# Kernel optimization log

Measured on AMD Instinct MI355X. Metric: run time of the kernel, lower is better.

## Reference

```python
import jax, jax.numpy as jnp
import numpy as np

# Spike nonlinearity with straight-through surrogate gradient
# fwd: z = (v_scaled > 0); bwd: dz/dv = clamp(1 - |v_scaled|, min=0)
@jax.custom_vjp
def spike(v_scaled):
    return (v_scaled > 0).astype(v_scaled.dtype)

def _spike_fwd(v_scaled):
    return spike(v_scaled), v_scaled

def _spike_bwd(v_scaled, g):
    return (g * jnp.maximum(1.0 - jnp.abs(v_scaled), 0.0),)

spike.defvjp(_spike_fwd, _spike_bwd)

_H = np.array([-0.00285825, 0.09859432, 0.07954306, 0.08560576, 0.0910411, 0.10557652,
               0.04608637, 0.07096123, 0.01989892, 0.03412642, 0.03321506, 0.01300904,
               -0.02348068, 0.06102338, -0.00509757, 0.00051896], dtype=np.float32)
_D = np.array([0.04908372, -0.00948576, 0.00083943, 0.07961489, 0.08128168, 0.02395899,
               0.05197346, 0.01595683, 0.02185501, 0.01893722, 0.0074682, -0.00088913,
               0.01660369, 0.00298292, 0.0071363, 0.00279426], dtype=np.float32)
_T = np.array([0.20153396, -0.01304637, -0.19541621, 0.19903184, 0.1529713, -0.00479887,
               0.07102165, 0.02109929, 0.01368383, -0.00360851, -0.01454873, -0.03991705,
               -0.00440092, -0.06122432, -0.02989412, -0.04975629], dtype=np.float32)


def setup_inputs() -> dict:
    key = jax.random.key(0)
    x = jax.random.normal(key, (64, 1024, 1024), dtype=jnp.float32)
    return {
        "x": x,
        "h": jnp.asarray(_H),
        "d": jnp.asarray(_D),
        "T": jnp.asarray(_T),
    }


def reference(x, h, d, T):
    signs = jax.lax.stop_gradient(jnp.sign(x))  # detached in original
    x_abs = jnp.abs(x)

    def step(carry, hdT):
        v, z, out = carry
        ht, dt, Tt = hdT
        v = v - z * ht
        v_scaled = (v - Tt) / (jnp.abs(v) + 1.0)
        z = spike(v_scaled)
        out = out + z * dt
        return (v, z, out), None

    init = (x_abs, jnp.zeros_like(x_abs), jnp.zeros_like(x_abs))
    (_, _, out), _ = jax.lax.scan(step, init, (h, d, T))  # K=16 steps
    return out * signs
```

## Files before the change

kernel.cpp:

```cpp
#include <hip/hip_runtime.h>


__device__ __forceinline__ float snn_elem(float xe,
                                          const float* __restrict__ hh,
                                          const float* __restrict__ dd,
                                          const float* __restrict__ TT) {
    float v = fabsf(xe);
    float z   = (v > TT[0]) ? 1.0f : 0.0f;
    float acc = z * dd[0];
#pragma unroll
    for (int t = 1; t < 16; ++t) {
        v   = fmaf(-z, hh[t], v);
        z   = (v > TT[t]) ? 1.0f : 0.0f;
        acc = fmaf(z, dd[t], acc);
    }
    float s = (xe > 0.0f) ? 1.0f : ((xe < 0.0f) ? -1.0f : 0.0f);
    return acc * s;
}

__global__ __launch_bounds__(256) void snn_scan_kernel(
    const float* __restrict__ x,
    const float* __restrict__ h,
    const float* __restrict__ d,
    const float* __restrict__ T,
    float* __restrict__ out,
    int n4, int n) {
    float hh[16], dd[16], TT[16];
#pragma unroll
    for (int t = 0; t < 16; ++t) {
        hh[t] = h[t];
        dd[t] = d[t];
        TT[t] = T[t];
    }

    const int stride = gridDim.x * blockDim.x;
    const float4* __restrict__ x4 = reinterpret_cast<const float4*>(x);
    float4* __restrict__ o4       = reinterpret_cast<float4*>(out);

    for (int i = blockIdx.x * blockDim.x + threadIdx.x; i < n4; i += stride) {
        float4 xv = x4[i];
        float4 ov;
        ov.x = snn_elem(xv.x, hh, dd, TT);
        ov.y = snn_elem(xv.y, hh, dd, TT);
        ov.z = snn_elem(xv.z, hh, dd, TT);
        ov.w = snn_elem(xv.w, hh, dd, TT);
        o4[i] = ov;
    }

    for (int i = n4 * 4 + blockIdx.x * blockDim.x + threadIdx.x; i < n;
         i += stride) {
        out[i] = snn_elem(x[i], hh, dd, TT);
    }
}

extern "C" void kernel_launch(void* const* d_in, const int* in_sizes, int n_in,
                              void* d_out, int out_size, void* d_ws, size_t ws_size,
                              hipStream_t stream) {
    const float* x = (const float*)d_in[0];
    const float* h = (const float*)d_in[1];
    const float* d = (const float*)d_in[2];
    const float* T = (const float*)d_in[3];
    float* out     = (float*)d_out;

    const int n  = in_sizes[0];
    const int n4 = n / 4;

    const int block = 256;
    int grid = 2048;
    const int needed = (n4 + block - 1) / block;
    if (grid > needed) grid = needed > 0 ? needed : 1;

    snn_scan_kernel<<<grid, block, 0, stream>>>(x, h, d, T, out, n4, n);
}
```

Baseline: 144.6 us.

## Software-pipeline grid-stride loads with 4-deep prefetch and nontemporal stores

Restructures the grid-stride loop so each thread issues four float4 loads ahead and computes on the previous batch while the next loads are in flight. Outputs are written with nontemporal stores to avoid polluting cache. The sign multiply is replaced by a sign-bit XOR with a zero check. Adds register pressure and a separate tail path for elements outside the full-step region.

```diff
diff --git a/kernel.cpp b/kernel.cpp
--- a/kernel.cpp
+++ b/kernel.cpp
@@ -1,5 +1,7 @@
 #include <hip/hip_runtime.h>
 
+
+typedef float f32x4 __attribute__((ext_vector_type(4)));
 
 __device__ __forceinline__ float snn_elem(float xe,
                                           const float* __restrict__ hh,
@@ -14,8 +16,19 @@
         z   = (v > TT[t]) ? 1.0f : 0.0f;
         acc = fmaf(z, dd[t], acc);
     }
-    float s = (xe > 0.0f) ? 1.0f : ((xe < 0.0f) ? -1.0f : 0.0f);
-    return acc * s;
+    unsigned ai = __float_as_uint(acc) ^ (__float_as_uint(xe) & 0x80000000u);
+    float r = __uint_as_float(ai);
+    return (xe == 0.0f) ? 0.0f : r;
+}
+
+__device__ __forceinline__ f32x4 snn_vec4(f32x4 xv,
+                                          const float* __restrict__ hh,
+                                          const float* __restrict__ dd,
+                                          const float* __restrict__ TT) {
+    f32x4 ov;
+#pragma unroll
+    for (int e = 0; e < 4; ++e) ov[e] = snn_elem(xv[e], hh, dd, TT);
+    return ov;
 }
 
 __global__ __launch_bounds__(256) void snn_scan_kernel(
@@ -24,31 +37,47 @@
     const float* __restrict__ d,
     const float* __restrict__ T,
     float* __restrict__ out,
-    int n4, int n) {
+    int n4, int n4_full, int n) {
     float hh[16], dd[16], TT[16];
 #pragma unroll
-    for (int t = 0; t < 16; ++t) {
-        hh[t] = h[t];
-        dd[t] = d[t];
-        TT[t] = T[t];
+    for (int t = 0; t < 16; ++t) { hh[t] = h[t]; dd[t] = d[t]; TT[t] = T[t]; }
+
+    const f32x4* __restrict__ x4 = (const f32x4*)x;
+    f32x4* __restrict__ o4       = (f32x4*)out;
+
+    const int tid  = blockIdx.x * blockDim.x + threadIdx.x;
+    const int nt   = gridDim.x * blockDim.x;
+    const int step = nt * 4;
+
+    int base = tid;
+    if (base < n4_full) {
+        f32x4 c0 = x4[base];
+        f32x4 c1 = x4[base + nt];
+        f32x4 c2 = x4[base + 2 * nt];
+        f32x4 c3 = x4[base + 3 * nt];
+        int nb = base + step;
+        for (; nb < n4_full; nb += step) {
+            f32x4 p0 = x4[nb];
+            f32x4 p1 = x4[nb + nt];
+            f32x4 p2 = x4[nb + 2 * nt];
+            f32x4 p3 = x4[nb + 3 * nt];
+            __builtin_nontemporal_store(snn_vec4(c0, hh, dd, TT), o4 + base);
+            __builtin_nontemporal_store(snn_vec4(c1, hh, dd, TT), o4 + base + nt);
+            __builtin_nontemporal_store(snn_vec4(c2, hh, dd, TT), o4 + base + 2 * nt);
+            __builtin_nontemporal_store(snn_vec4(c3, hh, dd, TT), o4 + base + 3 * nt);
+            c0 = p0; c1 = p1; c2 = p2; c3 = p3;
+            base = nb;
+        }
+        __builtin_nontemporal_store(snn_vec4(c0, hh, dd, TT), o4 + base);
+        __builtin_nontemporal_store(snn_vec4(c1, hh, dd, TT), o4 + base + nt);
+        __builtin_nontemporal_store(snn_vec4(c2, hh, dd, TT), o4 + base + 2 * nt);
+        __builtin_nontemporal_store(snn_vec4(c3, hh, dd, TT), o4 + base + 3 * nt);
     }
 
-    const int stride = gridDim.x * blockDim.x;
-    const float4* __restrict__ x4 = reinterpret_cast<const float4*>(x);
-    float4* __restrict__ o4       = reinterpret_cast<float4*>(out);
-
-    for (int i = blockIdx.x * blockDim.x + threadIdx.x; i < n4; i += stride) {
-        float4 xv = x4[i];
-        float4 ov;
-        ov.x = snn_elem(xv.x, hh, dd, TT);
-        ov.y = snn_elem(xv.y, hh, dd, TT);
-        ov.z = snn_elem(xv.z, hh, dd, TT);
-        ov.w = snn_elem(xv.w, hh, dd, TT);
-        o4[i] = ov;
+    for (int i = n4_full + tid; i < n4; i += nt) {
+        __builtin_nontemporal_store(snn_vec4(x4[i], hh, dd, TT), o4 + i);
     }
-
-    for (int i = n4 * 4 + blockIdx.x * blockDim.x + threadIdx.x; i < n;
-         i += stride) {
+    for (int i = n4 * 4 + tid; i < n; i += nt) {
         out[i] = snn_elem(x[i], hh, dd, TT);
     }
 }
@@ -70,5 +99,9 @@
     const int needed = (n4 + block - 1) / block;
     if (grid > needed) grid = needed > 0 ? needed : 1;
 
-    snn_scan_kernel<<<grid, block, 0, stream>>>(x, h, d, T, out, n4, n);
+    const int nt      = grid * block;
+    const int step    = nt * 4;
+    const int n4_full = (n4 / step) * step;
+
+    snn_scan_kernel<<<grid, block, 0, stream>>>(x, h, d, T, out, n4, n4_full, n);
 }
```

Result: slower. 218.4 us (+51.1%).

## Replace per-element 16-step scan with piecewise-constant LUT built on device

Applied to the files above, without the earlier changes.

Adds a single-block kernel that finds every breakpoint in |x| where the 16-step spike pattern changes, by bisecting over float bit patterns. It sorts the breakpoints, stores the output value for each segment, and builds a coarse bin index for lookup. The apply kernel loads this table into shared memory, maps each element to its segment through a bin lookup plus a short linear search, and also double-buffers its float4 loads. This removes the serial per-element recurrence but adds a serialized build-kernel launch and shared-memory lookups, and it falls back to the direct scan if the segment count overflows.

```diff
diff --git a/kernel.cpp b/kernel.cpp
--- a/kernel.cpp
+++ b/kernel.cpp
@@ -1,55 +1,246 @@
 #include <hip/hip_runtime.h>
 
 
-__device__ __forceinline__ float snn_elem(float xe,
-                                          const float* __restrict__ hh,
+#define NSEG_MAX 512
+#define NBIN 2048
+#define WS_WORDS (2 + NSEG_MAX + NSEG_MAX + NBIN)
+
+__device__ __forceinline__ int predmask(float a, const float* __restrict__ hh,
+                                        const float* __restrict__ TT) {
+    float v = a, z = 0.0f;
+    int m = 0;
+#pragma unroll
+    for (int k = 0; k < 16; ++k) {
+        v = fmaf(-z, hh[k], v);
+        int zb = (v > TT[k]) ? 1 : 0;
+        z = zb ? 1.0f : 0.0f;
+        m |= zb << k;
+    }
+    return m;
+}
+
+__device__ __forceinline__ float scan_val(float a, const float* __restrict__ hh,
                                           const float* __restrict__ dd,
                                           const float* __restrict__ TT) {
-    float v = fabsf(xe);
-    float z   = (v > TT[0]) ? 1.0f : 0.0f;
-    float acc = z * dd[0];
-#pragma unroll
-    for (int t = 1; t < 16; ++t) {
-        v   = fmaf(-z, hh[t], v);
-        z   = (v > TT[t]) ? 1.0f : 0.0f;
-        acc = fmaf(z, dd[t], acc);
-    }
-    float s = (xe > 0.0f) ? 1.0f : ((xe < 0.0f) ? -1.0f : 0.0f);
-    return acc * s;
-}
-
-__global__ __launch_bounds__(256) void snn_scan_kernel(
-    const float* __restrict__ x,
-    const float* __restrict__ h,
-    const float* __restrict__ d,
-    const float* __restrict__ T,
-    float* __restrict__ out,
-    int n4, int n) {
+    float v = a, z = 0.0f, acc = 0.0f;
+#pragma unroll
+    for (int k = 0; k < 16; ++k) {
+        v = fmaf(-z, hh[k], v);
+        z = (v > TT[k]) ? 1.0f : 0.0f;
+        acc = fmaf(z, dd[k], acc);
+    }
+    return acc;
+}
+
+__global__ __launch_bounds__(1024) void snn_build_lut(
+    const float* __restrict__ h, const float* __restrict__ d,
+    const float* __restrict__ T, unsigned int* __restrict__ ws) {
+    __shared__ unsigned int segL[NSEG_MAX], segH[NSEG_MAX];
+    __shared__ int nseg, ovf;
+    const int tid = threadIdx.x;
+    const int NT = blockDim.x;
+
     float hh[16], dd[16], TT[16];
 #pragma unroll
+    for (int k = 0; k < 16; ++k) { hh[k] = h[k]; dd[k] = d[k]; TT[k] = T[k]; }
+
+    if (tid == 0) { segL[0] = 0u; segH[0] = 0x7F800000u; nseg = 1; ovf = 0; }
+    __syncthreads();
+
     for (int t = 0; t < 16; ++t) {
-        hh[t] = h[t];
-        dd[t] = d[t];
-        TT[t] = T[t];
-    }
-
-    const int stride = gridDim.x * blockDim.x;
+        int cnt = nseg;
+        __syncthreads();
+        for (int i = tid; i < cnt; i += NT) {
+            unsigned int L = segL[i], H = segH[i];
+            int pL = (predmask(__uint_as_float(L), hh, TT) >> t) & 1;
+            int pH = (predmask(__uint_as_float(H - 1u), hh, TT) >> t) & 1;
+            if (pL != pH) {
+                unsigned int lo = L, hi = H - 1u;
+                while (hi - lo > 2u) {
+                    unsigned int q = (hi - lo) >> 2;
+                    unsigned int m1 = lo + q, m2 = lo + 2u * q, m3 = lo + 3u * q;
+                    int p1 = (predmask(__uint_as_float(m1), hh, TT) >> t) & 1;
+                    int p2 = (predmask(__uint_as_float(m2), hh, TT) >> t) & 1;
+                    int p3 = (predmask(__uint_as_float(m3), hh, TT) >> t) & 1;
+                    if (p1) hi = m1;
+                    else if (p2) { lo = m1 + 1u; hi = m2; }
+                    else if (p3) { lo = m2 + 1u; hi = m3; }
+                    else lo = m3 + 1u;
+                }
+                while (lo < hi) {
+                    if ((predmask(__uint_as_float(lo), hh, TT) >> t) & 1) break;
+                    ++lo;
+                }
+                unsigned int astar = lo;
+                int k = atomicAdd(&nseg, 1);
+                if (k < NSEG_MAX) {
+                    segL[k] = astar;
+                    segH[k] = H;
+                    segH[i] = astar;
+                } else {
+                    ovf = 1;
+                }
+            }
+        }
+        __syncthreads();
+    }
+
+    int ns = (nseg > NSEG_MAX) ? NSEG_MAX : nseg;
+    for (int i = tid; i < NSEG_MAX; i += NT)
+        if (i >= ns) segL[i] = 0xFFFFFFFFu;
+    __syncthreads();
+
+    for (int k = 2; k <= NSEG_MAX; k <<= 1) {
+        for (int s = k >> 1; s > 0; s >>= 1) {
+            __syncthreads();
+            if (tid < NSEG_MAX / 2) {
+                int idx = ((tid / s) * (s << 1)) + (tid % s);
+                int part = idx | s;
+                bool up = ((idx & k) == 0);
+                unsigned int A = segL[idx], B = segL[part];
+                if (up ? (A > B) : (A < B)) { segL[idx] = B; segL[part] = A; }
+            }
+        }
+    }
+    __syncthreads();
+
+    for (int j = tid; j < ns; j += NT)
+        ws[2 + NSEG_MAX + j] =
+            __float_as_uint(scan_val(__uint_as_float(segL[j]), hh, dd, TT));
+
+    for (int b = tid; b < NBIN; b += NT) {
+        float blo = (float)b * (1.0f / (float)NBIN);
+        unsigned int tb = __float_as_uint(blo);
+        int lo = 0, hi = ns - 1, j = 0;
+        while (lo <= hi) {
+            int mid = (lo + hi) >> 1;
+            if (segL[mid] <= tb) { j = mid; lo = mid + 1; }
+            else hi = mid - 1;
+        }
+        ws[2 + 2 * NSEG_MAX + b] = (unsigned int)j;
+    }
+    for (int i = tid; i < NSEG_MAX; i += NT) ws[2 + i] = segL[i];
+    if (tid == 0) { ws[0] = (unsigned int)ns; ws[1] = (unsigned int)ovf; }
+}
+
+__device__ __forceinline__ float lut_elem(float xe, const unsigned int* bpS,
+                                          const float* valS,
+                                          const unsigned short* gsS, int ns,
+                                          bool ovf, const float* __restrict__ hh,
+                                          const float* __restrict__ dd,
+                                          const float* __restrict__ TT) {
+    unsigned int sb = __float_as_uint(xe) & 0x80000000u;
+    float r;
+    if (!ovf) {
+        unsigned int ab = __float_as_uint(xe) & 0x7FFFFFFFu;
+        float a = __uint_as_float(ab);
+        float as = fminf(a * (float)NBIN, (float)(NBIN - 1));
+        int b = (int)as;
+        int j = gsS[b];
+        while (j + 1 < ns && ab >= bpS[j + 1]) ++j;
+        r = valS[j];
+    } else {
+        r = scan_val(__uint_as_float(__float_as_uint(xe) & 0x7FFFFFFFu), hh, dd, TT);
+    }
+    float o = __uint_as_float(__float_as_uint(r) ^ sb);
+    return (xe == 0.0f) ? 0.0f : o;
+}
+
+__global__ __launch_bounds__(256) void snn_apply(
+    const float* __restrict__ x, const float* __restrict__ h,
+    const float* __restrict__ d, const float* __restrict__ T,
+    float* __restrict__ out, const unsigned int* __restrict__ ws,
+    int n8, int n4, int n) {
+    __shared__ unsigned int bpS[NSEG_MAX];
+    __shared__ float valS[NSEG_MAX];
+    __shared__ unsigned short gsS[NBIN];
+    __shared__ int nsS, ovfS;
+    const int tid = threadIdx.x;
+
+    float hh[16], dd[16], TT[16];
+#pragma unroll
+    for (int k = 0; k < 16; ++k) { hh[k] = h[k]; dd[k] = d[k]; TT[k] = T[k]; }
+
+    for (int i = tid; i < NSEG_MAX; i += 256) {
+        bpS[i] = ws[2 + i];
+        valS[i] = __uint_as_float(ws[2 + NSEG_MAX + i]);
+    }
+    for (int b = tid; b < NBIN; b += 256)
+        gsS[b] = (unsigned short)ws[2 + 2 * NSEG_MAX + b];
+    if (tid == 0) { nsS = (int)ws[0]; ovfS = (int)ws[1]; }
+    __syncthreads();
+    const int ns = nsS;
+    const bool ovf = (ovfS != 0);
+
     const float4* __restrict__ x4 = reinterpret_cast<const float4*>(x);
-    float4* __restrict__ o4       = reinterpret_cast<float4*>(out);
-
-    for (int i = blockIdx.x * blockDim.x + threadIdx.x; i < n4; i += stride) {
-        float4 xv = x4[i];
-        float4 ov;
-        ov.x = snn_elem(xv.x, hh, dd, TT);
-        ov.y = snn_elem(xv.y, hh, dd, TT);
-        ov.z = snn_elem(xv.z, hh, dd, TT);
-        ov.w = snn_elem(xv.w, hh, dd, TT);
+    float4* __restrict__ o4 = reinterpret_cast<float4*>(out);
+    const int gtid = blockIdx.x * blockDim.x + tid;
+    const int nt = gridDim.x * blockDim.x;
+
+#define APPLY4(vv)                                                              \
+    {                                                                           \
+        float4 ov;                                                              \
+        ov.x = lut_elem(vv.x, bpS, valS, gsS, ns, ovf, hh, dd, TT);             \
+        ov.y = lut_elem(vv.y, bpS, valS, gsS, ns, ovf, hh, dd, TT);             \
+        ov.z = lut_elem(vv.z, bpS, valS, gsS, ns, ovf, hh, dd, TT);             \
+        ov.w = lut_elem(vv.w, bpS, valS, gsS, ns, ovf, hh, dd, TT);             \
+        vv = ov;                                                                \
+    }
+
+    int i = gtid;
+    if (i < n8) {
+        float4 ca = x4[2 * i], cb = x4[2 * i + 1];
+        int nx = i + nt;
+        while (nx < n8) {
+            float4 pa = x4[2 * nx], pb = x4[2 * nx + 1];
+            APPLY4(ca); APPLY4(cb);
+            o4[2 * i] = ca; o4[2 * i + 1] = cb;
+            ca = pa; cb = pb;
+            i = nx; nx += nt;
+        }
+        APPLY4(ca); APPLY4(cb);
+        o4[2 * i] = ca; o4[2 * i + 1] = cb;
+    }
+    for (int j = n8 * 2 + gtid; j < n4; j += nt) {
+        float4 v = x4[j];
+        APPLY4(v);
+        o4[j] = v;
+    }
+    for (int j = n4 * 4 + gtid; j < n; j += nt)
+        out[j] = lut_elem(x[j], bpS, valS, gsS, ns, ovf, hh, dd, TT);
+#undef APPLY4
+}
+
+__global__ __launch_bounds__(256) void snn_direct(
+    const float* __restrict__ x, const float* __restrict__ h,
+    const float* __restrict__ d, const float* __restrict__ T,
+    float* __restrict__ out, int n4, int n) {
+    float hh[16], dd[16], TT[16];
+#pragma unroll
+    for (int k = 0; k < 16; ++k) { hh[k] = h[k]; dd[k] = d[k]; TT[k] = T[k]; }
+    const float4* __restrict__ x4 = reinterpret_cast<const float4*>(x);
+    float4* __restrict__ o4 = reinterpret_cast<float4*>(out);
+    const int gtid = blockIdx.x * blockDim.x + threadIdx.x;
+    const int nt = gridDim.x * blockDim.x;
+    for (int i = gtid; i < n4; i += nt) {
+        float4 v = x4[i], ov;
+        float* pi = &v.x;
+        float* po = &ov.x;
+#pragma unroll
+        for (int e = 0; e < 4; ++e) {
+            float xe = pi[e];
+            float acc = scan_val(fabsf(xe), hh, dd, TT);
+            unsigned int rb =
+                __float_as_uint(acc) ^ (__float_as_uint(xe) & 0x80000000u);
+            po[e] = (xe == 0.0f) ? 0.0f : __uint_as_float(rb);
+        }
         o4[i] = ov;
     }
-
-    for (int i = n4 * 4 + blockIdx.x * blockDim.x + threadIdx.x; i < n;
-         i += stride) {
-        out[i] = snn_elem(x[i], hh, dd, TT);
+    for (int j = n4 * 4 + gtid; j < n; j += nt) {
+        float xe = x[j];
+        float acc = scan_val(fabsf(xe), hh, dd, TT);
+        unsigned int rb = __float_as_uint(acc) ^ (__float_as_uint(xe) & 0x80000000u);
+        out[j] = (xe == 0.0f) ? 0.0f : __uint_as_float(rb);
     }
 }
 
@@ -60,15 +251,25 @@
     const float* h = (const float*)d_in[1];
     const float* d = (const float*)d_in[2];
     const float* T = (const float*)d_in[3];
-    float* out     = (float*)d_out;
-
-    const int n  = in_sizes[0];
+    float* out = (float*)d_out;
+
+    const int n = in_sizes[0];
     const int n4 = n / 4;
-
-    const int block = 256;
+    const int n8 = n / 8;
+
+    if (ws_size < (size_t)WS_WORDS * 4) {
+        int grid = 2048;
+        const int needed = (n4 + 255) / 256;
+        if (grid > needed) grid = needed > 0 ? needed : 1;
+        snn_direct<<<grid, 256, 0, stream>>>(x, h, d, T, out, n4, n);
+        return;
+    }
+
+    unsigned int* ws = (unsigned int*)d_ws;
+    snn_build_lut<<<1, 1024, 0, stream>>>(h, d, T, ws);
+
     int grid = 2048;
-    const int needed = (n4 + block - 1) / block;
+    const int needed = (n8 + 255) / 256;
     if (grid > needed) grid = needed > 0 ? needed : 1;
-
-    snn_scan_kernel<<<grid, block, 0, stream>>>(x, h, d, T, out, n4, n);
-}
+    snn_apply<<<grid, 256, 0, stream>>>(x, h, d, T, out, ws, n8, n4, n);
+}
```

New measurement: 283.1 us. +95.8%, slower.
